# Optimization experiments

Hardware: AMD Instinct MI355X
Metric: run time of the kernel (lower is better)

Reference implementation:

```python
import jax, jax.numpy as jnp
import numpy as np

COUPLING = 1.0
DT = 1.0
ATTR = 1.0
AFF_SCALE = 0.25          # feedback_affinity_scale
ALPHA_FAC = 0.25 * 1.0    # feedback_alpha_scale * alpha_scale (eval mode)
CHUNK = 256               # coupling_chunk_size
C_IN = 3                  # input_channels


def _pairwise_coupling(theta, spikes):
    """All-pairs vector Kuramoto coupling within one channel group.
    theta: [B, n, D], spikes: [B, n] -> [B, n, D]
    Chunked over receiver nodes i (lax.scan) to avoid [B,n,n,D] materialization."""
    B, n, D = theta.shape
    rng = jnp.clip(spikes.max(axis=1, keepdims=True) - spikes.min(axis=1, keepdims=True), 1e-6)  # [B,1]
    nchunks = n // CHUNK
    theta_i = theta.reshape(B, nchunks, CHUNK, D).transpose(1, 0, 2, 3)   # [nc,B,C,D]
    spike_i = spikes.reshape(B, nchunks, CHUNK).transpose(1, 0, 2)        # [nc,B,C]

    def body(_, xs):
        ti, si = xs                                              # [B,C,D], [B,C]
        nd = jnp.abs(si[:, :, None] - spikes[:, None, :]) / rng[:, :, None]   # [B,C,n]
        aff = AFF_SCALE * (1.0 - nd)
        alpha = ALPHA_FAC * nd
        # sin(theta_j - theta_i - alpha_ij): [B,C,n,D]
        phase = jnp.sin(theta[:, None, :, :] - ti[:, :, None, :] - alpha[..., None])
        out = (COUPLING / n) * jnp.sum(aff[..., None] * phase, axis=2)        # [B,C,D]
        return None, out

    _, outs = jax.lax.scan(body, None, (theta_i, spike_i))       # [nc,B,C,D]
    return outs.transpose(1, 0, 2, 3).reshape(B, n, D)


def _channel_wise_coupling(theta, spikes):
    """HWC flatten: channel c occupies nodes c, c+C, c+2C, ..."""
    B, N, D = theta.shape
    nc = N // C_IN
    th = theta.reshape(B, nc, C_IN, D).transpose(2, 0, 1, 3)     # [C_IN,B,nc,D]
    sp = spikes.reshape(B, nc, C_IN).transpose(2, 0, 1)          # [C_IN,B,nc]
    outs = jax.vmap(_pairwise_coupling)(th, sp)                  # [C_IN,B,nc,D]
    return outs.transpose(1, 2, 0, 3).reshape(B, N, D)


def setup_inputs() -> dict:
    key = jax.random.key(0)
    k1, k2, k3 = jax.random.split(key, 3)
    B, N, D = 4, 12288, 4
    return {
        "theta_prev": jax.random.normal(k1, (B, N, D), dtype=jnp.float32),
        "gamma_prev": jax.random.normal(k2, (B, N, D), dtype=jnp.float32),
        "affinity": jax.random.uniform(k3, (B, N), dtype=jnp.float32),
    }


def reference(theta_prev, gamma_prev, affinity):
    coupling_term = _channel_wise_coupling(theta_prev, affinity)
    theta_dot = ATTR * (gamma_prev - theta_prev) + coupling_term
    theta_next = theta_prev + DT * theta_dot
    # torch.nn.functional.normalize: x / max(||x||_2, eps)
    norm = jnp.maximum(jnp.linalg.norm(theta_next, axis=-1, keepdims=True), 1e-6)
    return theta_next / norm
```

## Files before the change

kernel.cpp:

```cpp
#include <hip/hip_runtime.h>
#include <math.h>

#define BATCH 4
#define NN    12288
#define CIN   3
#define NC    4096
#define NG    12
#define NB    128
#define HSTR  9
#define PSZ   (4 * NB * 8)

#define SC_OFF 0
#define P_OFF  64
#define H2_OFF (P_OFF + 192 * PSZ)

__launch_bounds__(256)
__global__ void k_stats(const float* __restrict__ spikes, float* __restrict__ ws) {
    int g = blockIdx.x, b = g / CIN, c = g % CIN;
    const float4* row = (const float4*)(spikes + b * NN);
    int tid = threadIdx.x, lane = tid & 63, w = tid >> 6;
    float mn = 1e30f, mx = -1e30f;
    #pragma unroll
    for (int q = 0; q < 12; ++q) {
        int f = tid + q * 256;
        float4 v4 = row[f];
        float e[4] = {v4.x, v4.y, v4.z, v4.w};
        int r = (4 * f) % 3;
        int j0 = (c - r + 3) % 3;
        mn = fminf(mn, e[j0]); mx = fmaxf(mx, e[j0]);
        if (j0 + 3 < 4) { mn = fminf(mn, e[j0 + 3]); mx = fmaxf(mx, e[j0 + 3]); }
    }
    #pragma unroll
    for (int off = 32; off; off >>= 1) {
        mn = fminf(mn, __shfl_down(mn, off));
        mx = fmaxf(mx, __shfl_down(mx, off));
    }
    __shared__ float smn[4], smx[4];
    if (lane == 0) { smn[w] = mn; smx[w] = mx; }
    __syncthreads();
    if (tid == 0) {
        float m0 = fminf(fminf(smn[0], smn[1]), fminf(smn[2], smn[3]));
        float m1 = fmaxf(fmaxf(smx[0], smx[1]), fmaxf(smx[2], smx[3]));
        float scale = 0.25f / fmaxf(m1 - m0, 1e-6f);
        ws[SC_OFF + g * 2]     = scale;
        ws[SC_OFF + g * 2 + 1] = m0 * scale;
    }
}

__launch_bounds__(256)
__global__ void k_hist(const float* __restrict__ spikes,
                       const float* __restrict__ theta,
                       float* __restrict__ ws) {
    __shared__ float lh[4 * NB * HSTR];
    int blk = blockIdx.x, g = blk >> 4, chunk = blk & 15;
    int b = g / CIN, c = g % CIN;
    int tid = threadIdx.x;
    #pragma unroll
    for (int q = 0; q < 18; ++q) lh[tid + q * 256] = 0.f;
    float scale = ws[SC_OFF + g * 2], amin = ws[SC_OFF + g * 2 + 1];
    __syncthreads();

    int k = chunk * 256 + tid;
    int v = b * NN + k * CIN + c;
    float a = spikes[v] * scale;
    int bb = (int)((a - amin) * (4.0f * NB));
    bb = bb < 0 ? 0 : (bb > NB - 1 ? NB - 1 : bb);
    float sa, ca; __sincosf(a, &sa, &ca);
    float4 th = ((const float4*)theta)[v];
    float thv[4] = {th.x, th.y, th.z, th.w};
    #pragma unroll
    for (int d = 0; d < 4; ++d) {
        float sth, cth; __sincosf(thv[d], &sth, &cth);
        float sf = fmaf(cth, sa,  sth * ca);
        float cf = fmaf(-sth, sa, cth * ca);
        float sp = fmaf(-cth, sa, sth * ca);
        float cq = fmaf(sth, sa,  cth * ca);
        float* h = lh + (d * NB + bb) * HSTR;
        atomicAdd(h + 0, sf);      atomicAdd(h + 1, cf);
        atomicAdd(h + 2, a * sf);  atomicAdd(h + 3, a * cf);
        atomicAdd(h + 4, sp);      atomicAdd(h + 5, cq);
        atomicAdd(h + 6, a * sp);  atomicAdd(h + 7, a * cq);
    }
    __syncthreads();

    float* P = ws + P_OFF + (size_t)blk * PSZ;
    #pragma unroll
    for (int q = 0; q < 16; ++q) {
        int o = tid + q * 256;
        P[o] = lh[(o >> 3) * HSTR + (o & 7)];
    }
}

__launch_bounds__(256)
__global__ void k_mscan(float* __restrict__ ws) {
    __shared__ float lh[NB * HSTR];
    int gd = blockIdx.x, g = gd >> 2, d = gd & 3;
    int tid = threadIdx.x, lane = tid & 63, w = tid >> 6;

    const float* Pg = ws + P_OFF + (size_t)(g * 16) * PSZ + d * NB * 8;
    #pragma unroll
    for (int q = 0; q < 4; ++q) {
        int o = tid + q * 256;
        float s = 0.f;
        #pragma unroll
        for (int p = 0; p < 16; ++p) s += Pg[(size_t)p * PSZ + o];
        lh[(o >> 3) * HSTR + (o & 7)] = s;
    }
    __syncthreads();

    #pragma unroll
    for (int p = 0; p < 2; ++p) {
        int ch = w * 2 + p;
        float x0 = lh[(lane * 2 + 0) * HSTR + ch];
        float x1 = lh[(lane * 2 + 1) * HSTR + ch];
        float i0 = x0, i1 = i0 + x1;
        float incl = i1;
        #pragma unroll
        for (int off = 1; off < 64; off <<= 1) {
            float o = __shfl_up(incl, off);
            if (lane >= off) incl += o;
        }
        float ebt = incl - i1;
        lh[(lane * 2 + 0) * HSTR + ch] = ebt + i0;
        lh[(lane * 2 + 1) * HSTR + ch] = ebt + i1;
    }
    __syncthreads();

    float* H2 = ws + H2_OFF + (size_t)gd * (NB * 8);
    #pragma unroll
    for (int q = 0; q < 4; ++q) {
        int o = tid + q * 256;
        H2[o] = lh[(o >> 3) * HSTR + (o & 7)];
    }
}

__launch_bounds__(256)
__global__ void k_apply(const float* __restrict__ spikes,
                        const float* __restrict__ theta,
                        const float* __restrict__ gamma,
                        const float* __restrict__ ws,
                        float* __restrict__ out) {
    int blk = blockIdx.x, g = blk >> 4, chunk = blk & 15;
    int b = g / CIN, c = g % CIN;
    int tid = threadIdx.x;
    float scale = ws[SC_OFF + g * 2], amin = ws[SC_OFF + g * 2 + 1];
    int k = chunk * 256 + tid;
    int v = b * NN + k * CIN + c;
    float a = spikes[v] * scale;
    int bb = (int)((a - amin) * (4.0f * NB));
    bb = bb < 0 ? 0 : (bb > NB - 1 ? NB - 1 : bb);
    float sa, ca; __sincosf(a, &sa, &ca);
    float4 th = ((const float4*)theta)[v];
    float4 gm = ((const float4*)gamma)[v];
    float thv[4] = {th.x, th.y, th.z, th.w};
    float cp[4];
    #pragma unroll
    for (int d = 0; d < 4; ++d) {
        float sth, cth; __sincosf(thv[d], &sth, &cth);
        float sf = fmaf(cth, sa,  sth * ca);
        float cf = fmaf(-sth, sa, cth * ca);
        float sp = fmaf(-cth, sa, sth * ca);
        float cq = fmaf(sth, sa,  cth * ca);
        const float4* H4 = (const float4*)(ws + H2_OFF + (size_t)(g * 4 + d) * (NB * 8));
        float4 Plo = H4[bb * 2];
        float4 Phi = H4[bb * 2 + 1];
        float4 T   = H4[(NB - 1) * 2 + 1];
        float lowS = fmaf(0.25f - a, Plo.x, Plo.z);
        float lowC = fmaf(0.25f - a, Plo.y, Plo.w);
        float lower = cf * lowS - sf * lowC;
        float S4 = T.x - Phi.x, S5 = T.y - Phi.y;
        float S6 = T.z - Phi.z, S7 = T.w - Phi.w;
        float upS = fmaf(0.25f + a, S4, -S6);
        float upC = fmaf(0.25f + a, S5, -S7);
        float upper = cq * upS - sp * upC;
        cp[d] = (lower + upper) * (1.0f / (float)NC);
    }
    float tx = gm.x + cp[0], ty = gm.y + cp[1];
    float tz = gm.z + cp[2], tw = gm.w + cp[3];
    float nrm = sqrtf(tx * tx + ty * ty + tz * tz + tw * tw);
    float inv = 1.0f / fmaxf(nrm, 1e-6f);
    ((float4*)out)[v] = make_float4(tx * inv, ty * inv, tz * inv, tw * inv);
}

extern "C" void kernel_launch(void* const* d_in, const int* in_sizes, int n_in,
                              void* d_out, int out_size, void* d_ws, size_t ws_size,
                              hipStream_t stream) {
    const float* theta  = (const float*)d_in[0];
    const float* gamma  = (const float*)d_in[1];
    const float* spikes = (const float*)d_in[2];
    float* out = (float*)d_out;
    float* ws  = (float*)d_ws;

    hipLaunchKernelGGL(k_stats, dim3(NG),      dim3(256), 0, stream, spikes, ws);
    hipLaunchKernelGGL(k_hist,  dim3(NG * 16), dim3(256), 0, stream, spikes, theta, ws);
    hipLaunchKernelGGL(k_mscan, dim3(NG * 4),  dim3(256), 0, stream, ws);
    hipLaunchKernelGGL(k_apply, dim3(NG * 16), dim3(256), 0, stream,
                       spikes, theta, gamma, ws, out);
}
```

Before: 80.03 us.

## Fuse stats, histogram, scan and apply into one cooperative kernel with grid syncs

Merges the four launches into a single cooperative kernel of 192 blocks that uses grid.sync between the histogram, scan and apply phases. Each block recomputes the per-group min/max itself rather than reading it from a separate stats kernel. The per-node sin/cos terms are kept in registers between phases so they are not recomputed. This removes launch gaps and redundant work, at the cost of two grid-wide barriers and a cooperative-launch requirement.

```diff
diff --git a/kernel.cpp b/kernel.cpp
--- a/kernel.cpp
+++ b/kernel.cpp
@@ -1,5 +1,8 @@
 #include <hip/hip_runtime.h>
+#include <hip/hip_cooperative_groups.h>
 #include <math.h>
+
+namespace cg = cooperative_groups;
 
 #define BATCH 4
 #define NN    12288
@@ -10,22 +13,35 @@
 #define HSTR  9
 #define PSZ   (4 * NB * 8)
 
-#define SC_OFF 0
-#define P_OFF  64
-#define H2_OFF (P_OFF + 192 * PSZ)
+#define P_OFF  0
+#define H2_OFF (192 * PSZ)
 
 __launch_bounds__(256)
-__global__ void k_stats(const float* __restrict__ spikes, float* __restrict__ ws) {
-    int g = blockIdx.x, b = g / CIN, c = g % CIN;
+__global__ void k_coop(const float* __restrict__ spikes,
+                       const float* __restrict__ theta,
+                       const float* __restrict__ gamma,
+                       float* __restrict__ ws,
+                       float* __restrict__ out) {
+    cg::grid_group grid = cg::this_grid();
+    __shared__ float lh[4 * NB * HSTR];
+    __shared__ float smn[4], smx[4];
+    __shared__ float uScale, uAmin;
+
+    int blk = blockIdx.x, g = blk >> 4, chunk = blk & 15;
+    int b = g / CIN, c = g % CIN;
+    int tid = threadIdx.x, lane = tid & 63, w = tid >> 6;
+
+    #pragma unroll
+    for (int q = 0; q < 18; ++q) lh[tid + q * 256] = 0.f;
+
     const float4* row = (const float4*)(spikes + b * NN);
-    int tid = threadIdx.x, lane = tid & 63, w = tid >> 6;
     float mn = 1e30f, mx = -1e30f;
     #pragma unroll
     for (int q = 0; q < 12; ++q) {
         int f = tid + q * 256;
         float4 v4 = row[f];
         float e[4] = {v4.x, v4.y, v4.z, v4.w};
-        int r = (4 * f) % 3;
+        int r  = (4 * f) % 3;
         int j0 = (c - r + 3) % 3;
         mn = fminf(mn, e[j0]); mx = fmaxf(mx, e[j0]);
         if (j0 + 3 < 4) { mn = fminf(mn, e[j0 + 3]); mx = fmaxf(mx, e[j0 + 3]); }
@@ -35,30 +51,17 @@
         mn = fminf(mn, __shfl_down(mn, off));
         mx = fmaxf(mx, __shfl_down(mx, off));
     }
-    __shared__ float smn[4], smx[4];
     if (lane == 0) { smn[w] = mn; smx[w] = mx; }
     __syncthreads();
     if (tid == 0) {
         float m0 = fminf(fminf(smn[0], smn[1]), fminf(smn[2], smn[3]));
         float m1 = fmaxf(fmaxf(smx[0], smx[1]), fmaxf(smx[2], smx[3]));
         float scale = 0.25f / fmaxf(m1 - m0, 1e-6f);
-        ws[SC_OFF + g * 2]     = scale;
-        ws[SC_OFF + g * 2 + 1] = m0 * scale;
+        uScale = scale;
+        uAmin  = m0 * scale;
     }
-}
-
-__launch_bounds__(256)
-__global__ void k_hist(const float* __restrict__ spikes,
-                       const float* __restrict__ theta,
-                       float* __restrict__ ws) {
-    __shared__ float lh[4 * NB * HSTR];
-    int blk = blockIdx.x, g = blk >> 4, chunk = blk & 15;
-    int b = g / CIN, c = g % CIN;
-    int tid = threadIdx.x;
-    #pragma unroll
-    for (int q = 0; q < 18; ++q) lh[tid + q * 256] = 0.f;
-    float scale = ws[SC_OFF + g * 2], amin = ws[SC_OFF + g * 2 + 1];
     __syncthreads();
+    float scale = uScale, amin = uAmin;
 
     int k = chunk * 256 + tid;
     int v = b * NN + k * CIN + c;
@@ -68,18 +71,19 @@
     float sa, ca; __sincosf(a, &sa, &ca);
     float4 th = ((const float4*)theta)[v];
     float thv[4] = {th.x, th.y, th.z, th.w};
+    float sf[4], cf[4], sp[4], cq[4];
     #pragma unroll
     for (int d = 0; d < 4; ++d) {
         float sth, cth; __sincosf(thv[d], &sth, &cth);
-        float sf = fmaf(cth, sa,  sth * ca);
-        float cf = fmaf(-sth, sa, cth * ca);
-        float sp = fmaf(-cth, sa, sth * ca);
-        float cq = fmaf(sth, sa,  cth * ca);
+        sf[d] = fmaf(cth, sa,  sth * ca);
+        cf[d] = fmaf(-sth, sa, cth * ca);
+        sp[d] = fmaf(-cth, sa, sth * ca);
+        cq[d] = fmaf(sth, sa,  cth * ca);
         float* h = lh + (d * NB + bb) * HSTR;
-        atomicAdd(h + 0, sf);      atomicAdd(h + 1, cf);
-        atomicAdd(h + 2, a * sf);  atomicAdd(h + 3, a * cf);
-        atomicAdd(h + 4, sp);      atomicAdd(h + 5, cq);
-        atomicAdd(h + 6, a * sp);  atomicAdd(h + 7, a * cq);
+        atomicAdd(h + 0, sf[d]);      atomicAdd(h + 1, cf[d]);
+        atomicAdd(h + 2, a * sf[d]);  atomicAdd(h + 3, a * cf[d]);
+        atomicAdd(h + 4, sp[d]);      atomicAdd(h + 5, cq[d]);
+        atomicAdd(h + 6, a * sp[d]);  atomicAdd(h + 7, a * cq[d]);
     }
     __syncthreads();
 
@@ -89,90 +93,64 @@
         int o = tid + q * 256;
         P[o] = lh[(o >> 3) * HSTR + (o & 7)];
     }
-}
 
-__launch_bounds__(256)
-__global__ void k_mscan(float* __restrict__ ws) {
-    __shared__ float lh[NB * HSTR];
-    int gd = blockIdx.x, g = gd >> 2, d = gd & 3;
-    int tid = threadIdx.x, lane = tid & 63, w = tid >> 6;
+    grid.sync();
 
-    const float* Pg = ws + P_OFF + (size_t)(g * 16) * PSZ + d * NB * 8;
-    #pragma unroll
-    for (int q = 0; q < 4; ++q) {
-        int o = tid + q * 256;
-        float s = 0.f;
+    if (blk < 48) {
+        int gg = blk >> 2, d = blk & 3;
+        const float* Pg = ws + P_OFF + (size_t)(gg * 16) * PSZ + d * NB * 8;
         #pragma unroll
-        for (int p = 0; p < 16; ++p) s += Pg[(size_t)p * PSZ + o];
-        lh[(o >> 3) * HSTR + (o & 7)] = s;
+        for (int q = 0; q < 4; ++q) {
+            int o = tid + q * 256;
+            float s = 0.f;
+            #pragma unroll
+            for (int p = 0; p < 16; ++p) s += Pg[(size_t)p * PSZ + o];
+            lh[(o >> 3) * HSTR + (o & 7)] = s;
+        }
+        __syncthreads();
+        #pragma unroll
+        for (int p = 0; p < 2; ++p) {
+            int ch = w * 2 + p;
+            float x0 = lh[(lane * 2 + 0) * HSTR + ch];
+            float x1 = lh[(lane * 2 + 1) * HSTR + ch];
+            float i0 = x0, i1 = i0 + x1;
+            float incl = i1;
+            #pragma unroll
+            for (int off = 1; off < 64; off <<= 1) {
+                float o = __shfl_up(incl, off);
+                if (lane >= off) incl += o;
+            }
+            float ebt = incl - i1;
+            lh[(lane * 2 + 0) * HSTR + ch] = ebt + i0;
+            lh[(lane * 2 + 1) * HSTR + ch] = ebt + i1;
+        }
+        __syncthreads();
+        float* H2 = ws + H2_OFF + (size_t)blk * (NB * 8);
+        #pragma unroll
+        for (int q = 0; q < 4; ++q) {
+            int o = tid + q * 256;
+            H2[o] = lh[(o >> 3) * HSTR + (o & 7)];
+        }
     }
-    __syncthreads();
 
-    #pragma unroll
-    for (int p = 0; p < 2; ++p) {
-        int ch = w * 2 + p;
-        float x0 = lh[(lane * 2 + 0) * HSTR + ch];
-        float x1 = lh[(lane * 2 + 1) * HSTR + ch];
-        float i0 = x0, i1 = i0 + x1;
-        float incl = i1;
-        #pragma unroll
-        for (int off = 1; off < 64; off <<= 1) {
-            float o = __shfl_up(incl, off);
-            if (lane >= off) incl += o;
-        }
-        float ebt = incl - i1;
-        lh[(lane * 2 + 0) * HSTR + ch] = ebt + i0;
-        lh[(lane * 2 + 1) * HSTR + ch] = ebt + i1;
-    }
-    __syncthreads();
+    grid.sync();
 
-    float* H2 = ws + H2_OFF + (size_t)gd * (NB * 8);
-    #pragma unroll
-    for (int q = 0; q < 4; ++q) {
-        int o = tid + q * 256;
-        H2[o] = lh[(o >> 3) * HSTR + (o & 7)];
-    }
-}
-
-__launch_bounds__(256)
-__global__ void k_apply(const float* __restrict__ spikes,
-                        const float* __restrict__ theta,
-                        const float* __restrict__ gamma,
-                        const float* __restrict__ ws,
-                        float* __restrict__ out) {
-    int blk = blockIdx.x, g = blk >> 4, chunk = blk & 15;
-    int b = g / CIN, c = g % CIN;
-    int tid = threadIdx.x;
-    float scale = ws[SC_OFF + g * 2], amin = ws[SC_OFF + g * 2 + 1];
-    int k = chunk * 256 + tid;
-    int v = b * NN + k * CIN + c;
-    float a = spikes[v] * scale;
-    int bb = (int)((a - amin) * (4.0f * NB));
-    bb = bb < 0 ? 0 : (bb > NB - 1 ? NB - 1 : bb);
-    float sa, ca; __sincosf(a, &sa, &ca);
-    float4 th = ((const float4*)theta)[v];
     float4 gm = ((const float4*)gamma)[v];
-    float thv[4] = {th.x, th.y, th.z, th.w};
     float cp[4];
     #pragma unroll
     for (int d = 0; d < 4; ++d) {
-        float sth, cth; __sincosf(thv[d], &sth, &cth);
-        float sf = fmaf(cth, sa,  sth * ca);
-        float cf = fmaf(-sth, sa, cth * ca);
-        float sp = fmaf(-cth, sa, sth * ca);
-        float cq = fmaf(sth, sa,  cth * ca);
         const float4* H4 = (const float4*)(ws + H2_OFF + (size_t)(g * 4 + d) * (NB * 8));
         float4 Plo = H4[bb * 2];
         float4 Phi = H4[bb * 2 + 1];
         float4 T   = H4[(NB - 1) * 2 + 1];
         float lowS = fmaf(0.25f - a, Plo.x, Plo.z);
         float lowC = fmaf(0.25f - a, Plo.y, Plo.w);
-        float lower = cf * lowS - sf * lowC;
+        float lower = cf[d] * lowS - sf[d] * lowC;
         float S4 = T.x - Phi.x, S5 = T.y - Phi.y;
         float S6 = T.z - Phi.z, S7 = T.w - Phi.w;
         float upS = fmaf(0.25f + a, S4, -S6);
         float upC = fmaf(0.25f + a, S5, -S7);
-        float upper = cq * upS - sp * upC;
+        float upper = cq[d] * upS - sp[d] * upC;
         cp[d] = (lower + upper) * (1.0f / (float)NC);
     }
     float tx = gm.x + cp[0], ty = gm.y + cp[1];
@@ -191,9 +169,8 @@
     float* out = (float*)d_out;
     float* ws  = (float*)d_ws;
 
-    hipLaunchKernelGGL(k_stats, dim3(NG),      dim3(256), 0, stream, spikes, ws);
-    hipLaunchKernelGGL(k_hist,  dim3(NG * 16), dim3(256), 0, stream, spikes, theta, ws);
-    hipLaunchKernelGGL(k_mscan, dim3(NG * 4),  dim3(256), 0, stream, ws);
-    hipLaunchKernelGGL(k_apply, dim3(NG * 16), dim3(256), 0, stream,
-                       spikes, theta, gamma, ws, out);
+    void* args[] = {(void*)&spikes, (void*)&theta, (void*)&gamma,
+                    (void*)&ws, (void*)&out};
+    hipLaunchCooperativeKernel((void*)k_coop, dim3(NG * 16), dim3(256),
+                               args, 0, stream);
 }
```

After: 138.4 us. 1.73x slower.
